# Kernel tuning notes

Hardware: AMD Instinct MI355X
Metric: run time of the kernel (lower is better)

## Reference

```python
import jax, jax.numpy as jnp
import numpy as np

IN_FEATURES = 4096
OUT_FEATURES = 4096
H_ROWS = 4096
TILE_H = 256  # weight row-tile / input col-tile size in Linear_CIM
TILE_W = 64   # weight col-tile size in Linear_CIM


def setup_inputs() -> dict:
    key = jax.random.key(0)
    kx, kw, kb = jax.random.split(key, 3)
    x = jax.random.normal(kx, (H_ROWS, IN_FEATURES), dtype=jnp.float32)
    # kaiming_uniform_(a=sqrt(5)) on (out, in) weight -> bound = 1/sqrt(in_features)
    bound = 1.0 / np.sqrt(IN_FEATURES)
    weight = jax.random.uniform(kw, (OUT_FEATURES, IN_FEATURES), dtype=jnp.float32,
                                minval=-bound, maxval=bound)
    bias = jax.random.uniform(kb, (OUT_FEATURES,), dtype=jnp.float32,
                              minval=-bound, maxval=bound)
    return {"x": x, "weight": weight, "bias": bias}


def reference(x, weight, bias):
    # Faithful translation of Linear_CIM(input, weight.T, bias).
    # In the original, the loop over weight row-tiles (i) and the loop over
    # input column-tiles (w) are INDEPENDENT, so every input 256-block is
    # multiplied against every weight 256-row block. Mathematically:
    #   out[:, :num_w*64] = (sum_w X_w) @ (sum_i Wt_i)   (+ bias everywhere)
    wt = weight.T                      # (in_features, out_features)
    h, win = x.shape
    out_f = wt.shape[1]
    num_vec = win // TILE_H
    num_h = wt.shape[0] // TILE_H
    num_w = out_f // TILE_W
    xs = x[:, :num_vec * TILE_H].reshape(h, num_vec, TILE_H).sum(axis=1)      # (h, 256)
    ws = wt[:num_h * TILE_H].reshape(num_h, TILE_H, out_f).sum(axis=0)        # (256, out_f)
    cols = num_w * TILE_W
    out = jnp.zeros((h, out_f), dtype=x.dtype)
    out = out.at[:, :cols].set(xs @ ws[:, :cols])
    return out + bias
```

## Files before the change

kernel.cpp:

```cpp
#include <hip/hip_runtime.h>

#define H_ROWS 4096
#define IN_F   4096
#define OUT_F  4096

typedef __bf16 bf16;
typedef __bf16 bf16x4 __attribute__((ext_vector_type(4)));
typedef __bf16 bf16x8 __attribute__((ext_vector_type(8)));
typedef float  f32x4  __attribute__((ext_vector_type(4)));

__global__ __launch_bounds__(256) void reduce_kernel(
    const float* __restrict__ x, const float* __restrict__ w,
    bf16* __restrict__ xs, bf16* __restrict__ wsT)
{
    __shared__ float lds[1024];
    const int bid = blockIdx.x;
    const float* __restrict__ src = (bid & 1) ? w : x;
    bf16* __restrict__ dst = (bid & 1) ? wsT : xs;
    const int r   = bid >> 1;
    const int tid = threadIdx.x;

    const float4* __restrict__ s = (const float4*)src + r * (IN_F / 4);
    float4 a0 = s[tid];
    float4 a1 = s[tid + 256];
    float4 a2 = s[tid + 512];
    float4 a3 = s[tid + 768];
    float4 acc;
    acc.x = (a0.x + a1.x) + (a2.x + a3.x);
    acc.y = (a0.y + a1.y) + (a2.y + a3.y);
    acc.z = (a0.z + a1.z) + (a2.z + a3.z);
    acc.w = (a0.w + a1.w) + (a2.w + a3.w);

    ((float4*)lds)[tid] = acc;
    __syncthreads();

    if (tid < 64) {
        float4 b0 = ((const float4*)lds)[tid];
        float4 b1 = ((const float4*)lds)[tid + 64];
        float4 b2 = ((const float4*)lds)[tid + 128];
        float4 b3 = ((const float4*)lds)[tid + 192];
        float4 t;
        t.x = (b0.x + b1.x) + (b2.x + b3.x);
        t.y = (b0.y + b1.y) + (b2.y + b3.y);
        t.z = (b0.z + b1.z) + (b2.z + b3.z);
        t.w = (b0.w + b1.w) + (b2.w + b3.w);
        bf16x4 o;
        o[0] = (bf16)t.x; o[1] = (bf16)t.y; o[2] = (bf16)t.z; o[3] = (bf16)t.w;
        *(bf16x4*)(dst + r * 256 + tid * 4) = o;
    }
}

__global__ __launch_bounds__(256) void gemm_bt_kernel(
    const bf16* __restrict__ A, const bf16* __restrict__ B,
    const float* __restrict__ bias, float* __restrict__ out)
{
    __shared__ bf16 As[2][128 * 32];
    __shared__ bf16 Bs[2][128 * 32];

    const int m0   = blockIdx.y * 128;
    const int n0   = blockIdx.x * 128;
    const int tid  = threadIdx.x;
    const int lane = tid & 63;
    const int w    = tid >> 6;
    const int wm   = (w & 1) * 64;
    const int wn   = (w >> 1) * 64;
    const int l15  = lane & 15;
    const int quad = lane >> 4;

    #define STAGE(b, kk)                                                      \
    {                                                                         \
        const int k0 = (kk) * 32;                                             \
        _Pragma("unroll")                                                     \
        for (int c = 0; c < 2; ++c) {                                         \
            const int chunk = c * 256 + tid;                                  \
            const int row   = chunk >> 2;                                     \
            const int kc    = chunk & 3;                                      \
            const bf16* ga = A + (m0 + row) * 256 + k0 + kc * 8;              \
            const bf16* gb = B + (n0 + row) * 256 + k0 + kc * 8;              \
            __builtin_amdgcn_global_load_lds(                                 \
                (const __attribute__((address_space(1))) void*)ga,            \
                (__attribute__((address_space(3))) void*)(As[b] + chunk * 8), \
                16, 0, 0);                                                    \
            __builtin_amdgcn_global_load_lds(                                 \
                (const __attribute__((address_space(1))) void*)gb,            \
                (__attribute__((address_space(3))) void*)(Bs[b] + chunk * 8), \
                16, 0, 0);                                                    \
        }                                                                     \
    }

    f32x4 acc[4][4] = {};

    STAGE(0, 0);

    int buf = 0;
    for (int kk = 0; kk < 8; ++kk) {
        __syncthreads();
        if (kk < 7) STAGE(buf ^ 1, kk + 1);

        bf16x8 af[4], bfr[4];
        #pragma unroll
        for (int t = 0; t < 4; ++t) {
            af[t]  = *(const bf16x8*)(As[buf] + (wm + t * 16 + l15) * 32 + quad * 8);
            bfr[t] = *(const bf16x8*)(Bs[buf] + (wn + t * 16 + l15) * 32 + quad * 8);
        }
        #pragma unroll
        for (int mt = 0; mt < 4; ++mt)
            #pragma unroll
            for (int nt = 0; nt < 4; ++nt)
                acc[mt][nt] = __builtin_amdgcn_mfma_f32_16x16x32_bf16(
                    af[mt], bfr[nt], acc[mt][nt], 0, 0, 0);
        buf ^= 1;
    }
    #undef STAGE

    #pragma unroll
    for (int nt = 0; nt < 4; ++nt) {
        const int col = n0 + wn + nt * 16 + l15;
        const float bv = bias[col];
        #pragma unroll
        for (int mt = 0; mt < 4; ++mt) {
            const int rbase = m0 + wm + mt * 16 + quad * 4;
            #pragma unroll
            for (int r = 0; r < 4; ++r)
                out[(rbase + r) * OUT_F + col] = acc[mt][nt][r] + bv;
        }
    }
}

extern "C" void kernel_launch(void* const* d_in, const int* in_sizes, int n_in,
                              void* d_out, int out_size, void* d_ws, size_t ws_size,
                              hipStream_t stream)
{
    const float* x      = (const float*)d_in[0];
    const float* weight = (const float*)d_in[1];
    const float* bias   = (const float*)d_in[2];
    float* out = (float*)d_out;

    bf16* xs  = (bf16*)d_ws;
    bf16* wsT = xs + 4096 * 256;

    reduce_kernel<<<8192, 256, 0, stream>>>(x, weight, xs, wsT);
    gemm_bt_kernel<<<dim3(32, 32), 256, 0, stream>>>(xs, wsT, bias, out);
}
```

Measured before the change: 189.2 us.

## Stage GEMM epilogue through LDS for coalesced float4 stores; split reduce launches

The GEMM epilogue now writes each 16-row slab of accumulators (plus bias) into shared memory, then reads it back as float4 vectors so each output row segment is stored with coalesced 16-byte writes instead of scattered 4-byte stores. Shared memory is reused as a flat buffer for this. The combined reduce kernel is split into two launches, one for x and one for weight, which removes the per-block source selection but adds a kernel launch. The epilogue adds eight block-wide barriers and extra LDS traffic.

Result: faster. 181.0 us (-4.3%).

```diff
diff --git a/kernel.cpp b/kernel.cpp
--- a/kernel.cpp
+++ b/kernel.cpp
@@ -9,15 +9,11 @@
 typedef __bf16 bf16x8 __attribute__((ext_vector_type(8)));
 typedef float  f32x4  __attribute__((ext_vector_type(4)));
 
-__global__ __launch_bounds__(256) void reduce_kernel(
-    const float* __restrict__ x, const float* __restrict__ w,
-    bf16* __restrict__ xs, bf16* __restrict__ wsT)
+__global__ __launch_bounds__(256) void reduce_half_kernel(
+    const float* __restrict__ src, bf16* __restrict__ dst)
 {
     __shared__ float lds[1024];
-    const int bid = blockIdx.x;
-    const float* __restrict__ src = (bid & 1) ? w : x;
-    bf16* __restrict__ dst = (bid & 1) ? wsT : xs;
-    const int r   = bid >> 1;
+    const int r   = blockIdx.x;
     const int tid = threadIdx.x;
 
     const float4* __restrict__ s = (const float4*)src + r * (IN_F / 4);
@@ -54,8 +50,9 @@
     const bf16* __restrict__ A, const bf16* __restrict__ B,
     const float* __restrict__ bias, float* __restrict__ out)
 {
-    __shared__ bf16 As[2][128 * 32];
-    __shared__ bf16 Bs[2][128 * 32];
+    __shared__ bf16 smem[16384];
+    bf16* As = smem;
+    bf16* Bs = smem + 8192;
 
     const int m0   = blockIdx.y * 128;
     const int n0   = blockIdx.x * 128;
@@ -79,11 +76,11 @@
             const bf16* gb = B + (n0 + row) * 256 + k0 + kc * 8;              \
             __builtin_amdgcn_global_load_lds(                                 \
                 (const __attribute__((address_space(1))) void*)ga,            \
-                (__attribute__((address_space(3))) void*)(As[b] + chunk * 8), \
+                (__attribute__((address_space(3))) void*)(As + (b) * 4096 + chunk * 8), \
                 16, 0, 0);                                                    \
             __builtin_amdgcn_global_load_lds(                                 \
                 (const __attribute__((address_space(1))) void*)gb,            \
-                (__attribute__((address_space(3))) void*)(Bs[b] + chunk * 8), \
+                (__attribute__((address_space(3))) void*)(Bs + (b) * 4096 + chunk * 8), \
                 16, 0, 0);                                                    \
         }                                                                     \
     }
@@ -100,8 +97,8 @@
         bf16x8 af[4], bfr[4];
         #pragma unroll
         for (int t = 0; t < 4; ++t) {
-            af[t]  = *(const bf16x8*)(As[buf] + (wm + t * 16 + l15) * 32 + quad * 8);
-            bfr[t] = *(const bf16x8*)(Bs[buf] + (wn + t * 16 + l15) * 32 + quad * 8);
+            af[t]  = *(const bf16x8*)(As + buf * 4096 + (wm + t * 16 + l15) * 32 + quad * 8);
+            bfr[t] = *(const bf16x8*)(Bs + buf * 4096 + (wn + t * 16 + l15) * 32 + quad * 8);
         }
         #pragma unroll
         for (int mt = 0; mt < 4; ++mt)
@@ -113,16 +110,31 @@
     }
     #undef STAGE
 
+    float* sc = (float*)smem;
+    const int w1 = w & 1;
+    float bv[4];
     #pragma unroll
-    for (int nt = 0; nt < 4; ++nt) {
-        const int col = n0 + wn + nt * 16 + l15;
-        const float bv = bias[col];
+    for (int nt = 0; nt < 4; ++nt) bv[nt] = bias[n0 + wn + nt * 16 + l15];
+
+    #pragma unroll
+    for (int mt = 0; mt < 4; ++mt) {
+        __syncthreads();
         #pragma unroll
-        for (int mt = 0; mt < 4; ++mt) {
-            const int rbase = m0 + wm + mt * 16 + quad * 4;
+        for (int nt = 0; nt < 4; ++nt) {
+            const int col = wn + nt * 16 + l15;
             #pragma unroll
             for (int r = 0; r < 4; ++r)
-                out[(rbase + r) * OUT_F + col] = acc[mt][nt][r] + bv;
+                sc[(w1 * 16 + quad * 4 + r) * 132 + col] = acc[mt][nt][r] + bv[nt];
+        }
+        __syncthreads();
+        #pragma unroll
+        for (int i = 0; i < 4; ++i) {
+            const int id   = i * 256 + tid;
+            const int lrow = id >> 5;
+            const int cc   = id & 31;
+            f32x4 v = *(const f32x4*)(sc + lrow * 132 + cc * 4);
+            *(f32x4*)(out + (m0 + (lrow >> 4) * 64 + mt * 16 + (lrow & 15)) * OUT_F
+                      + n0 + cc * 4) = v;
         }
     }
 }
@@ -139,6 +151,7 @@
     bf16* xs  = (bf16*)d_ws;
     bf16* wsT = xs + 4096 * 256;
 
-    reduce_kernel<<<8192, 256, 0, stream>>>(x, weight, xs, wsT);
+    reduce_half_kernel<<<4096, 256, 0, stream>>>(x, xs);
+    reduce_half_kernel<<<4096, 256, 0, stream>>>(weight, wsT);
     gemm_bt_kernel<<<dim3(32, 32), 256, 0, stream>>>(xs, wsT, bias, out);
 }
```
